# Kernel tuning notes

Hardware: AMD Instinct MI355X
Metric: run time of the kernel (lower is better)

Reference implementation:

```python
import jax, jax.numpy as jnp
import numpy as np

K, D = 512, 256
NUM_CLASSES, SHARED_KEYS = 10, 10
B, H, W = 32, 64, 64
TRAINING = True


def setup_inputs() -> dict:
    key = jax.random.key(0)
    k1, k2, k3 = jax.random.split(key, 3)
    z_e_x = jax.random.normal(k1, (B, D, H, W), dtype=jnp.float32)
    labels = jax.random.randint(k2, (B,), 0, NUM_CLASSES)
    # nn.Embedding weight initialized uniform(-1/K, 1/K)
    codebook = jax.random.uniform(k3, (K, D), minval=-1.0 / K, maxval=1.0 / K,
                                  dtype=jnp.float32)
    return {"z_e_x": z_e_x, "codebook": codebook, "labels": labels}


def _irrelevant_regions(labels_flat, k, num_classes, n_shared, training):
    # uniform partition of the first K - n_shared codes over the classes
    uniform = jnp.round(jnp.linspace(-0.5, num_classes - 0.51, k - n_shared))  # [K-Ns]
    irrel = uniform[None, :] != labels_flat[:, None].astype(uniform.dtype)     # [N, K-Ns]
    n = labels_flat.shape[0]
    if training:
        tail = jnp.ones((n, n_shared), dtype=bool)   # TRAIN: shared keys masked out
    else:
        tail = jnp.zeros((n, n_shared), dtype=bool)
    return jnp.concatenate([irrel, tail], axis=1)    # [N, K]


def reference(z_e_x, codebook, labels):
    x = jnp.transpose(z_e_x, (0, 2, 3, 1))           # [B,H,W,D]
    xf = x.reshape(-1, D)                            # [N,D], N=B*H*W
    labels_flat = jnp.repeat(labels, H * W)          # [N]

    irrel = _irrelevant_regions(labels_flat, K, NUM_CLASSES, SHARED_KEYS, TRAINING)

    cb_sqr = jnp.sum(codebook * codebook, axis=1)                      # [K]
    in_sqr = jnp.sum(xf * xf, axis=1, keepdims=True)                   # [N,1]
    distances = in_sqr + cb_sqr[None, :] - 2.0 * (xf @ codebook.T)     # [N,K]
    distances = jnp.where(irrel, jnp.inf, distances)

    idx = jnp.argmin(distances, axis=1)                                # [N]

    codes = codebook[idx].reshape(x.shape)                             # [B,H,W,D]
    # straight-through path (detached codebook in torch)
    z_q = x + jax.lax.stop_gradient(codes - x)
    z_q_x = jnp.transpose(z_q, (0, 3, 1, 2))                           # [B,D,H,W]
    # non-detached codebook lookup path
    z_q_bar = codebook[jax.lax.stop_gradient(idx)].reshape(x.shape)
    z_q_x_bar = jnp.transpose(z_q_bar, (0, 3, 1, 2))                   # [B,D,H,W]
    return (z_q_x, z_q_x_bar)
```

## Files before the change

### kernel.cpp

```cpp
#include <hip/hip_runtime.h>


#define D       256
#define KCODES  512
#define HW      4096
#define BATCH   32
#define NPTS    (BATCH * HW)
#define WPW     13
#define PF      8

__constant__ int c_cls_start[11] = {0, 51, 101, 151, 201, 251, 301, 352, 402, 452, 502};

__global__ __launch_bounds__(256) void prep_kernel(const float* __restrict__ cb,
                                                   float* __restrict__ cbT,
                                                   float* __restrict__ cbs) {
    const int k = blockIdx.x;
    const int d = threadIdx.x;
    float v = cb[k * D + d];
    cbT[(size_t)d * KCODES + k] = v;
    __shared__ double red[256];
    red[d] = (double)v * (double)v;
    __syncthreads();
    for (int s = 128; s > 0; s >>= 1) {
        if (d < s) red[d] += red[d + s];
        __syncthreads();
    }
    if (d == 0) cbs[k] = (float)red[0];
}

__global__ __launch_bounds__(256, 8) void vq_kernel(const float* __restrict__ z,
                                                    const int* __restrict__ labels,
                                                    const float* __restrict__ cbT,
                                                    const float* __restrict__ cbs,
                                                    float* __restrict__ out) {
    const int lane = threadIdx.x & 63;
    const int w    = __builtin_amdgcn_readfirstlane(threadIdx.x >> 6);
    const int b    = blockIdx.x >> 6;
    const int hw   = ((blockIdx.x & 63) << 6) | lane;
    const int lab  = __builtin_amdgcn_readfirstlane(labels[b]);
    const int c0   = c_cls_start[lab];
    const int cnt  = c_cls_start[lab + 1] - c0;
    const int kbase = c0 + w * WPW;
    const int myn   = min(WPW, cnt - w * WPW);

    const float* __restrict__ xp = z + (size_t)b * (D * HW) + hw;

    float acc[WPW];
#pragma unroll
    for (int j = 0; j < WPW; ++j) acc[j] = 0.0f;

    double xsq = 0.0;

    float xb[PF];
#pragma unroll
    for (int i = 0; i < PF; ++i) xb[i] = xp[(size_t)i * HW];

    for (int d = 0; d < D; d += PF) {
        float xn[PF];
#pragma unroll
        for (int i = 0; i < PF; ++i) {
            int dn = (d + PF + i) & (D - 1);
            xn[i] = xp[(size_t)dn * HW];
        }
#pragma unroll
        for (int i = 0; i < PF; ++i) {
            const float* __restrict__ wd = cbT + (size_t)(d + i) * KCODES + kbase;
            const float x = xb[i];
            xsq = fma((double)x, (double)x, xsq);
#pragma unroll
            for (int j = 0; j < WPW; ++j)
                acc[j] = fmaf(x, wd[j], acc[j]);
        }
#pragma unroll
        for (int i = 0; i < PF; ++i) xb[i] = xn[i];
    }

    const float insq = (float)xsq;
    float best = __builtin_inff();
    int bi = kbase;
#pragma unroll
    for (int j = 0; j < WPW; ++j) {
        if (j < myn) {
            float T    = insq + cbs[kbase + j];
            float dist = fmaf(-2.0f, acc[j], T);
            if (dist < best) { best = dist; bi = kbase + j; }
        }
    }

    __shared__ float sd[4][64];
    __shared__ int   si[4][64];
    sd[w][lane] = best;
    si[w][lane] = bi;
    __syncthreads();
    float fb = sd[0][lane];
    int   fi = si[0][lane];
#pragma unroll
    for (int w2 = 1; w2 < 4; ++w2) {
        float dv = sd[w2][lane];
        if (dv < fb) { fb = dv; fi = si[w2][lane]; }
    }

    float* __restrict__ o0 = out + (size_t)b * (D * HW) + hw;
    float* __restrict__ o1 = o0 + (size_t)NPTS * D;
    const int d0 = w * 64;
#pragma unroll 8
    for (int d = d0; d < d0 + 64; ++d) {
        float v = cbT[(size_t)d * KCODES + fi];
        __builtin_nontemporal_store(v, o0 + (size_t)d * HW);
        __builtin_nontemporal_store(v, o1 + (size_t)d * HW);
    }
}

extern "C" void kernel_launch(void* const* d_in, const int* in_sizes, int n_in,
                              void* d_out, int out_size, void* d_ws, size_t ws_size,
                              hipStream_t stream) {
    const float* z      = (const float*)d_in[0];
    const float* cb     = (const float*)d_in[1];
    const int*   labels = (const int*)d_in[2];
    float* out = (float*)d_out;

    float* cbT = (float*)d_ws;
    float* cbs = cbT + (size_t)D * KCODES;

    hipLaunchKernelGGL(prep_kernel, dim3(KCODES), dim3(D), 0, stream, cb, cbT, cbs);
    hipLaunchKernelGGL(vq_kernel, dim3(NPTS / 64), dim3(256), 0, stream,
                       z, labels, cbT, cbs, out);
}
```

Baseline: 393.4 us.

## Split argmin and output emission into separate kernels with vectorized 16-byte stores

The fused kernel is split in two. The argmin kernel now writes only the per-point code index to a global workspace buffer. A new emit kernel reads four indices per lane, gathers the codebook values and writes both outputs with 128-bit nontemporal stores instead of scalar stores. The aim is wider, more efficient writes for the store-bound output phase, at the cost of an extra kernel launch and an index round-trip through global memory.

```diff
diff --git a/kernel.cpp b/kernel.cpp
--- a/kernel.cpp
+++ b/kernel.cpp
@@ -8,6 +8,8 @@
 #define NPTS    (BATCH * HW)
 #define WPW     13
 #define PF      8
+
+typedef float fx4 __attribute__((ext_vector_type(4)));
 
 __constant__ int c_cls_start[11] = {0, 51, 101, 151, 201, 251, 301, 352, 402, 452, 502};
 
@@ -28,11 +30,11 @@
     if (d == 0) cbs[k] = (float)red[0];
 }
 
-__global__ __launch_bounds__(256, 8) void vq_kernel(const float* __restrict__ z,
-                                                    const int* __restrict__ labels,
-                                                    const float* __restrict__ cbT,
-                                                    const float* __restrict__ cbs,
-                                                    float* __restrict__ out) {
+__global__ __launch_bounds__(256, 8) void argmin_kernel(const float* __restrict__ z,
+                                                        const int* __restrict__ labels,
+                                                        const float* __restrict__ cbT,
+                                                        const float* __restrict__ cbs,
+                                                        int* __restrict__ fidxg) {
     const int lane = threadIdx.x & 63;
     const int w    = __builtin_amdgcn_readfirstlane(threadIdx.x >> 6);
     const int b    = blockIdx.x >> 6;
@@ -92,22 +94,44 @@
     sd[w][lane] = best;
     si[w][lane] = bi;
     __syncthreads();
-    float fb = sd[0][lane];
-    int   fi = si[0][lane];
+    if (w == 0) {
+        float fb = sd[0][lane];
+        int   fi = si[0][lane];
 #pragma unroll
-    for (int w2 = 1; w2 < 4; ++w2) {
-        float dv = sd[w2][lane];
-        if (dv < fb) { fb = dv; fi = si[w2][lane]; }
+        for (int w2 = 1; w2 < 4; ++w2) {
+            float dv = sd[w2][lane];
+            if (dv < fb) { fb = dv; fi = si[w2][lane]; }
+        }
+        fidxg[(size_t)b * HW + hw] = fi;
     }
+}
 
-    float* __restrict__ o0 = out + (size_t)b * (D * HW) + hw;
+__global__ __launch_bounds__(256) void emit_kernel(const int* __restrict__ fidxg,
+                                                   const float* __restrict__ cbT,
+                                                   float* __restrict__ out) {
+    const int lane = threadIdx.x & 63;
+    const int w    = threadIdx.x >> 6;
+    const int s    = blockIdx.x >> 2;
+    const int dq   = blockIdx.x & 3;
+    const int b    = s >> 4;
+    const int p0   = ((s & 15) << 8) | (lane << 2);
+
+    const int4 f = *(const int4*)(fidxg + (size_t)b * HW + p0);
+
+    float* __restrict__ o0 = out + (size_t)b * (D * HW) + p0;
     float* __restrict__ o1 = o0 + (size_t)NPTS * D;
-    const int d0 = w * 64;
-#pragma unroll 8
-    for (int d = d0; d < d0 + 64; ++d) {
-        float v = cbT[(size_t)d * KCODES + fi];
-        __builtin_nontemporal_store(v, o0 + (size_t)d * HW);
-        __builtin_nontemporal_store(v, o1 + (size_t)d * HW);
+    const int d0 = (dq << 6) | (w << 4);
+    const float* __restrict__ row = cbT + (size_t)d0 * KCODES;
+#pragma unroll 4
+    for (int d = d0; d < d0 + 16; ++d) {
+        fx4 v;
+        v.x = row[f.x];
+        v.y = row[f.y];
+        v.z = row[f.z];
+        v.w = row[f.w];
+        __builtin_nontemporal_store(v, (fx4*)(o0 + (size_t)d * HW));
+        __builtin_nontemporal_store(v, (fx4*)(o1 + (size_t)d * HW));
+        row += KCODES;
     }
 }
 
@@ -119,10 +143,13 @@
     const int*   labels = (const int*)d_in[2];
     float* out = (float*)d_out;
 
-    float* cbT = (float*)d_ws;
-    float* cbs = cbT + (size_t)D * KCODES;
+    float* cbT  = (float*)d_ws;
+    float* cbs  = cbT + (size_t)D * KCODES;
+    int*   fidx = (int*)(cbs + KCODES);
 
     hipLaunchKernelGGL(prep_kernel, dim3(KCODES), dim3(D), 0, stream, cb, cbT, cbs);
-    hipLaunchKernelGGL(vq_kernel, dim3(NPTS / 64), dim3(256), 0, stream,
-                       z, labels, cbT, cbs, out);
+    hipLaunchKernelGGL(argmin_kernel, dim3(NPTS / 64), dim3(256), 0, stream,
+                       z, labels, cbT, cbs, fidx);
+    hipLaunchKernelGGL(emit_kernel, dim3((NPTS / 256) * 4), dim3(256), 0, stream,
+                       fidx, cbT, out);
 }
```

After: 393.7 us. About the same (+0.1%).
